# Kernel optimization log

Measured on AMD Instinct MI355X. Metric: run time of the kernel, lower is better.

The kernel has to match this reference:

```python
import jax, jax.numpy as jnp
import numpy as np

B, T, D, H = 8, 1024, 512, 8
HD = D // H  # per-head hidden = embed_dim // n_head = 64
EPS = 1e-5


def setup_inputs() -> dict:
    key = jax.random.key(0)
    ks = jax.random.split(key, 8)
    x = jax.random.normal(ks[0], (B, T, D), dtype=jnp.float32)
    sc = 1.0 / np.sqrt(D)
    Wq = jax.random.normal(ks[1], (D, H * HD), dtype=jnp.float32) * sc
    Wk = jax.random.normal(ks[2], (D, H * HD), dtype=jnp.float32) * sc
    Wp = jax.random.normal(ks[3], (H * HD, D), dtype=jnp.float32) * sc
    bq = jnp.zeros((H * HD,), jnp.float32)
    bk = jnp.zeros((H * HD,), jnp.float32)
    bp = jnp.zeros((D,), jnp.float32)
    w_mlp = jax.random.normal(ks[4], (2 * HD,), dtype=jnp.float32) * 0.1
    ln_g = jnp.ones((D,), jnp.float32)
    ln_b = jnp.zeros((D,), jnp.float32)
    return {"x": x, "Wq": Wq, "bq": bq, "Wk": Wk, "bk": bk,
            "Wp": Wp, "bp": bp, "w_mlp": w_mlp, "ln_g": ln_g, "ln_b": ln_b}


def reference(x, Wq, bq, Wk, bk, Wp, bp, w_mlp, ln_g, ln_b):
    b, t, d = x.shape
    h, hd = H, HD
    # q/k projections, split into heads: [B,T,H,hd]
    qx = (x @ Wq + bq).reshape(b, t, h, hd)
    kx = (x @ Wk + bk).reshape(b, t, h, hd)
    # MLP score: tanh(concat(k_j, q_i) . w) == tanh(k_j.w[:hd] + q_i.w[hd:])
    k_s = jnp.einsum('bkhd,d->bkh', kx, w_mlp[:hd])   # [B,K,H]
    q_s = jnp.einsum('bqhd,d->bqh', qx, w_mlp[hd:])   # [B,Q,H]
    score = jnp.tanh(q_s[:, :, None, :] + k_s[:, None, :, :])  # [B,Q,K,H]
    attn = jax.nn.softmax(score, axis=2)  # softmax over k_len
    # values are the key projection kx (bmm(score, kx) in original)
    out = jnp.einsum('bqkh,bkhd->bqhd', attn, kx).reshape(b, t, h * hd)
    out = out @ Wp + bp  # output projection (dropout is identity at eval)
    # residual + LayerNorm
    y = x + out
    mu = jnp.mean(y, axis=-1, keepdims=True)
    var = jnp.var(y, axis=-1, keepdims=True)
    yn = (y - mu) * jax.lax.rsqrt(var + EPS)
    return yn * ln_g + ln_b
```

## Files before the change

kernel.cpp:

```cpp
#include <hip/hip_runtime.h>
#include <cstddef>

#define TT 1024
#define DDIM 512
#define HH 8
#define NND 128
#define NW 72

typedef __attribute__((ext_vector_type(8))) short bfrag;
typedef __attribute__((ext_vector_type(4))) float facc;

#define SC2   2.8853900817779268f
#define L2E   1.4426950408889634f

static __device__ __forceinline__ unsigned bfrne(float f) {
    unsigned u = __float_as_uint(f);
    return (u + 0x7fffu + ((u >> 16) & 1u)) >> 16;
}
static __device__ __forceinline__ unsigned pack2rne(float a, float b) {
    return bfrne(a) | (bfrne(b) << 16);
}
static __device__ __forceinline__ unsigned pack2hu(float a, float b) {
    return ((__float_as_uint(a) + 0x8000u) >> 16) |
           ((__float_as_uint(b) + 0x8000u) & 0xffff0000u);
}
static __device__ __forceinline__ void gl2lds16(const void* g, void* l) {
    __builtin_amdgcn_global_load_lds(
        (const __attribute__((address_space(1))) unsigned int*)g,
        (__attribute__((address_space(3))) unsigned int*)l, 16, 0, 0);
}
static __device__ __forceinline__ float wfun(float z2) {
    float t = __builtin_amdgcn_exp2f(z2);
    float r = __builtin_amdgcn_rcpf(t + 1.f);
    return __builtin_amdgcn_exp2f(fmaf(r, -2.f * L2E, L2E));
}

__global__ __launch_bounds__(256) void prepare_kernel(
    const float* __restrict__ x, const float* __restrict__ Wk,
    const float* __restrict__ Wp, const float* __restrict__ Wq,
    const float* __restrict__ bq, const float* __restrict__ wm,
    unsigned short* __restrict__ xb, unsigned short* __restrict__ WkT,
    unsigned short* __restrict__ WpT, unsigned short* __restrict__ vq2b,
    float* __restrict__ qsb2)
{
    const int bx = blockIdx.x, tid = threadIdx.x;
    if (bx < 2048) {
        const int lane = tid & 63, wave = tid >> 6;
        const int row = bx * 4 + wave;
        const float4* xr = (const float4*)(x + (size_t)row * DDIM);
        float4 x0 = xr[lane * 2], x1 = xr[lane * 2 + 1];
        uint4 st;
        st.x = pack2rne(x0.x, x0.y); st.y = pack2rne(x0.z, x0.w);
        st.z = pack2rne(x1.x, x1.y); st.w = pack2rne(x1.z, x1.w);
        int p = lane ^ (row & 7);
        *(uint4*)(xb + (size_t)row * DDIM + p * 8) = st;
    } else if (bx < 2176) {
        int idx = bx - 2048;
        const float* src = (idx & 64) ? Wp : Wk;
        unsigned short* dst = (idx & 64) ? WpT : WkT;
        idx &= 63;
        const int n0 = (idx & 7) * 64, k0 = (idx >> 3) * 64;
        __shared__ float sT[64][65];
        #pragma unroll
        for (int it = 0; it < 4; ++it) {
            int task = it * 256 + tid;
            int kr = task >> 4, c4 = (task & 15) * 4;
            float4 v = *(const float4*)(src + (size_t)(k0 + kr) * DDIM + n0 + c4);
            sT[kr][c4] = v.x; sT[kr][c4 + 1] = v.y; sT[kr][c4 + 2] = v.z; sT[kr][c4 + 3] = v.w;
        }
        __syncthreads();
        #pragma unroll
        for (int it = 0; it < 2; ++it) {
            int task = it * 256 + tid;
            int n = task >> 3, kg = task & 7;
            unsigned u[4];
            #pragma unroll
            for (int jj = 0; jj < 4; ++jj)
                u[jj] = pack2rne(sT[kg * 8 + jj * 2][n], sT[kg * 8 + jj * 2 + 1][n]);
            int p = ((k0 >> 3) + kg) ^ (n & 7);
            uint4 st; st.x = u[0]; st.y = u[1]; st.z = u[2]; st.w = u[3];
            *(uint4*)(dst + (size_t)(n0 + n) * DDIM + p * 8) = st;
        }
    } else {
        int idx = (bx - 2176) * 256 + tid;
        int h = idx >> 9, d = idx & 511;
        float s = 0.f;
        #pragma unroll 8
        for (int j = 0; j < 64; ++j)
            s = fmaf(Wq[(size_t)d * DDIM + h * 64 + j], wm[64 + j], s);
        vq2b[h * DDIM + d] = (unsigned short)bfrne(s * SC2);
        if (idx < HH) {
            float sb = 0.f;
            for (int j = 0; j < 64; ++j)
                sb = fmaf(bq[idx * 64 + j], wm[64 + j], sb);
            qsb2[idx] = sb * SC2;
        }
    }
}

__global__ __launch_bounds__(256) void gemm1_kernel(
    const unsigned short* __restrict__ A, const unsigned short* __restrict__ B,
    const float* __restrict__ bias, unsigned short* __restrict__ kxTg,
    float* __restrict__ ks2, const float* __restrict__ wm,
    const unsigned short* __restrict__ vq2b, const float* __restrict__ qsb2,
    float* __restrict__ qs2)
{
    __shared__ __align__(16) unsigned short smem[12288];
    unsigned short* sA = smem;
    unsigned short* sB = smem + 8192;
    const int tid = threadIdx.x, lane = tid & 63, wave = tid >> 6;
    const int l15 = lane & 15, quad = lane >> 4;
    const int h = blockIdx.x, row0 = blockIdx.y * 128;
    const int col0 = h * 64;

    facc acc[2][4]; facc accq[2];
    #pragma unroll
    for (int i = 0; i < 2; ++i) {
        #pragma unroll
        for (int j = 0; j < 4; ++j) { acc[i][j][0]=0.f; acc[i][j][1]=0.f; acc[i][j][2]=0.f; acc[i][j][3]=0.f; }
        accq[i][0]=0.f; accq[i][1]=0.f; accq[i][2]=0.f; accq[i][3]=0.f;
    }

    for (int k0 = 0; k0 < 512; k0 += 64) {
        #pragma unroll
        for (int it = 0; it < 4; ++it) {
            int g = it * 256 + tid;
            int r = g >> 3, kg = g & 7;
            gl2lds16(A + (size_t)(row0 + r) * 512 + k0 + kg * 8, &sA[g * 8]);
        }
        #pragma unroll
        for (int it = 0; it < 2; ++it) {
            int g = it * 256 + tid;
            int r = g >> 3, kg = g & 7;
            gl2lds16(B + (size_t)(col0 + r) * 512 + k0 + kg * 8, &sB[g * 8]);
        }
        __syncthreads();
        #pragma unroll
        for (int ks_ = 0; ks_ < 2; ++ks_) {
            int slot = (ks_ * 4 + quad) ^ (l15 & 7);
            bfrag a[2], b[4];
            #pragma unroll
            for (int i = 0; i < 2; ++i)
                a[i] = *(const bfrag*)&sA[(wave * 32 + i * 16 + l15) * 64 + slot * 8];
            #pragma unroll
            for (int nt = 0; nt < 4; ++nt)
                b[nt] = *(const bfrag*)&sB[(nt * 16 + l15) * 64 + slot * 8];
            bfrag bvq = *(const bfrag*)(vq2b + h * 512 + k0 + ks_ * 32 + quad * 8);
            #pragma unroll
            for (int i = 0; i < 2; ++i) {
                #pragma unroll
                for (int nt = 0; nt < 4; ++nt)
                    acc[i][nt] = __builtin_amdgcn_mfma_f32_16x16x32_bf16(a[i], b[nt], acc[i][nt], 0, 0, 0);
                accq[i] = __builtin_amdgcn_mfma_f32_16x16x32_bf16(a[i], bvq, accq[i], 0, 0, 0);
            }
        }
        __syncthreads();
    }

    const int bb = row0 >> 10, t0 = row0 & 1023;
    const float qsbh = qsb2[h];
    float bvv[4], wmv[4];
    #pragma unroll
    for (int nt = 0; nt < 4; ++nt) {
        bvv[nt] = bias[col0 + nt * 16 + l15];
        wmv[nt] = wm[nt * 16 + l15] * SC2;
    }
    float part[2][4];
    #pragma unroll
    for (int i = 0; i < 2; ++i)
        #pragma unroll
        for (int r = 0; r < 4; ++r) part[i][r] = 0.f;

    unsigned short* eT = smem;
    #pragma unroll
    for (int i = 0; i < 2; ++i) {
        int tr = wave * 32 + i * 16 + quad * 4;
        #pragma unroll
        for (int nt = 0; nt < 4; ++nt) {
            int col = nt * 16 + l15;
            float v0 = acc[i][nt][0] + bvv[nt], v1 = acc[i][nt][1] + bvv[nt];
            float v2 = acc[i][nt][2] + bvv[nt], v3 = acc[i][nt][3] + bvv[nt];
            part[i][0] = fmaf(wmv[nt], v0, part[i][0]);
            part[i][1] = fmaf(wmv[nt], v1, part[i][1]);
            part[i][2] = fmaf(wmv[nt], v2, part[i][2]);
            part[i][3] = fmaf(wmv[nt], v3, part[i][3]);
            *(unsigned*)&eT[col * 136 + tr]     = pack2rne(v0, v1);
            *(unsigned*)&eT[col * 136 + tr + 2] = pack2rne(v2, v3);
        }
    }
    #pragma unroll
    for (int i = 0; i < 2; ++i)
        #pragma unroll
        for (int r = 0; r < 4; ++r) {
            float p = part[i][r];
            p += __shfl_xor(p, 1); p += __shfl_xor(p, 2);
            p += __shfl_xor(p, 4); p += __shfl_xor(p, 8);
            if (l15 == 0) {
                size_t o = (size_t)(bb * HH + h) * TT + t0 + wave * 32 + i * 16 + quad * 4 + r;
                ks2[o] = p;
                qs2[o] = accq[i][r] + qsbh;
            }
        }
    __syncthreads();
    unsigned short* kxbase = kxTg + ((size_t)(bb * HH + h) * 64) * TT;
    #pragma unroll
    for (int it = 0; it < 4; ++it) {
        int task = it * 256 + tid;
        int col = task >> 4, seg = task & 15;
        uint4 v = *(const uint4*)&eT[col * 136 + seg * 8];
        int g = (t0 >> 3) + seg;
        int p = g ^ (col & 7);
        *(uint4*)(kxbase + (size_t)col * TT + p * 8) = v;
    }
}

__global__ __launch_bounds__(256) void attn_nodes_kernel(
    const unsigned short* __restrict__ kxTg, const float* __restrict__ qs2,
    const float* __restrict__ ks2, float* __restrict__ node_out,
    float* __restrict__ mn2, float* __restrict__ inv127)
{
    __shared__ __align__(16) unsigned short kxT[64 * 256];
    __shared__ float ksc[1024];
    __shared__ float redl[8];
    const int bh = blockIdx.x;
    const int tid = threadIdx.x, lane = tid & 63, wave = tid >> 6;
    const int l15 = lane & 15, quad = lane >> 4;

    ((float4*)ksc)[tid] = ((const float4*)(ks2 + (size_t)bh * TT))[tid];
    float4 q4 = ((const float4*)(qs2 + (size_t)bh * TT))[tid];
    float mn = fminf(fminf(q4.x, q4.y), fminf(q4.z, q4.w));
    float mx = fmaxf(fmaxf(q4.x, q4.y), fmaxf(q4.z, q4.w));
    #pragma unroll
    for (int off = 32; off > 0; off >>= 1) {
        mn = fminf(mn, __shfl_xor(mn, off));
        mx = fmaxf(mx, __shfl_xor(mx, off));
    }
    if (lane == 0) { redl[wave] = mn; redl[4 + wave] = mx; }
    __syncthreads();
    const float mnv = fminf(fminf(redl[0], redl[1]), fminf(redl[2], redl[3]));
    const float mxv = fmaxf(fmaxf(redl[4], redl[5]), fmaxf(redl[6], redl[7]));
    if (tid == 0) {
        mn2[bh] = mnv;
        inv127[bh] = 127.f / fmaxf(mxv - mnv, 1e-12f);
    }
    const float h2v = (mxv - mnv) * (1.f / 127.f);
    const float zA = mnv + (wave * 16 + l15) * h2v;
    const float zB = zA + 64.f * h2v;

    const unsigned short* kxbase = kxTg + (size_t)bh * 64 * TT;
    facc acc[2][4]; facc accZ[2];
    #pragma unroll
    for (int g = 0; g < 2; ++g) {
        #pragma unroll
        for (int i = 0; i < 4; ++i) { acc[g][i][0]=0.f; acc[g][i][1]=0.f; acc[g][i][2]=0.f; acc[g][i][3]=0.f; }
        accZ[g][0]=0.f; accZ[g][1]=0.f; accZ[g][2]=0.f; accZ[g][3]=0.f;
    }
    bfrag ones;
    #pragma unroll
    for (int j = 0; j < 8; ++j) ones[j] = (short)0x3F80;

    for (int ck = 0; ck < 4; ++ck) {
        #pragma unroll
        for (int it = 0; it < 8; ++it) {
            int g = it * 256 + tid;
            int d = g >> 5, j = g & 31;
            gl2lds16(kxbase + (size_t)d * TT + ck * 256 + j * 8, &kxT[g * 8]);
        }
        __syncthreads();
        #pragma unroll
        for (int kst = 0; kst < 8; ++kst) {
            const float* kvp = &ksc[ck * 256 + kst * 32 + quad * 8];
            float4 kv0 = *(const float4*)kvp;
            float4 kv1 = *(const float4*)(kvp + 4);
            int slot = (kst * 4 + quad) ^ (l15 & 7);
            bfrag bf_[4];
            #pragma unroll
            for (int dt = 0; dt < 4; ++dt)
                bf_[dt] = *(const bfrag*)&kxT[(dt * 16 + l15) * 256 + slot * 8];
            #pragma unroll
            for (int g = 0; g < 2; ++g) {
                float z = g ? zB : zA;
                union { unsigned u[4]; bfrag f; } afu;
                afu.u[0] = pack2hu(wfun(z + kv0.x), wfun(z + kv0.y));
                afu.u[1] = pack2hu(wfun(z + kv0.z), wfun(z + kv0.w));
                afu.u[2] = pack2hu(wfun(z + kv1.x), wfun(z + kv1.y));
                afu.u[3] = pack2hu(wfun(z + kv1.z), wfun(z + kv1.w));
                #pragma unroll
                for (int dt = 0; dt < 4; ++dt)
                    acc[g][dt] = __builtin_amdgcn_mfma_f32_16x16x32_bf16(afu.f, bf_[dt], acc[g][dt], 0, 0, 0);
                accZ[g] = __builtin_amdgcn_mfma_f32_16x16x32_bf16(afu.f, ones, accZ[g], 0, 0, 0);
            }
        }
        __syncthreads();
    }
    float* ob = node_out + (size_t)bh * NND * NW;
    #pragma unroll
    for (int g = 0; g < 2; ++g) {
        #pragma unroll
        for (int r = 0; r < 4; ++r) {
            int node = g * 64 + wave * 16 + quad * 4 + r;
            #pragma unroll
            for (int dt = 0; dt < 4; ++dt)
                ob[(size_t)node * NW + dt * 16 + l15] = acc[g][dt][r];
            if (l15 == 0) ob[(size_t)node * NW + 64] = accZ[g][r];
        }
    }
}

__global__ __launch_bounds__(256) void interp_kernel(
    const float* __restrict__ qs2, const float* __restrict__ node_out,
    const float* __restrict__ mn2, const float* __restrict__ inv127,
    unsigned short* __restrict__ attb)
{
    const int tid = threadIdx.x, lane = tid & 63, wave = tid >> 6;
    const int row = blockIdx.x * 4 + wave;
    const int b = row >> 10, t = row & 1023;
    const int hh2 = lane >> 5, dp = lane & 31;
    #pragma unroll
    for (int h0 = 0; h0 < 8; h0 += 2) {
        const int hh = h0 + hh2;
        const int bh = b * HH + hh;
        float qv = qs2[(size_t)bh * TT + t];
        float u = (qv - mn2[bh]) * inv127[bh];
        int i = (int)floorf(u) - 1;
        i = i < 0 ? 0 : (i > NND - 4 ? NND - 4 : i);
        float s = u - (float)i;
        float s1 = s - 1.f, s2 = s - 2.f, s3 = s - 3.f;
        float w0 = -s1 * s2 * s3 * (1.f / 6.f);
        float w1 = s * s2 * s3 * 0.5f;
        float w2 = -s * s1 * s3 * 0.5f;
        float w3 = s * s1 * s2 * (1.f / 6.f);
        const float* base = node_out + ((size_t)bh * NND + i) * NW;
        float2 v0 = *(const float2*)(base + 2 * dp);
        float2 v1 = *(const float2*)(base + NW + 2 * dp);
        float2 v2 = *(const float2*)(base + 2 * NW + 2 * dp);
        float2 v3 = *(const float2*)(base + 3 * NW + 2 * dp);
        float nx = w0 * v0.x + w1 * v1.x + w2 * v2.x + w3 * v3.x;
        float ny = w0 * v0.y + w1 * v1.y + w2 * v2.y + w3 * v3.y;
        float zz = w0 * base[64] + w1 * base[NW + 64] + w2 * base[2 * NW + 64] + w3 * base[3 * NW + 64];
        float rz = __builtin_amdgcn_rcpf(zz);
        unsigned pk = pack2rne(nx * rz, ny * rz);
        int col = hh * 64 + 2 * dp;
        int p = (col >> 3) ^ (row & 7);
        *(unsigned*)&attb[(size_t)row * DDIM + p * 8 + (col & 7)] = pk;
    }
}

__global__ __launch_bounds__(256) void gemm2_kernel(
    const unsigned short* __restrict__ A, const unsigned short* __restrict__ B,
    const float* __restrict__ bias, const float* __restrict__ x,
    unsigned short* __restrict__ yb)
{
    __shared__ __align__(16) unsigned short smem[12288];
    unsigned short* sA = smem;
    unsigned short* sB = smem + 8192;
    const int tid = threadIdx.x, lane = tid & 63, wave = tid >> 6;
    const int l15 = lane & 15, quad = lane >> 4;
    const int col0 = blockIdx.x * 64, row0 = blockIdx.y * 128;

    facc acc[2][4];
    #pragma unroll
    for (int i = 0; i < 2; ++i)
        #pragma unroll
        for (int j = 0; j < 4; ++j) { acc[i][j][0]=0.f; acc[i][j][1]=0.f; acc[i][j][2]=0.f; acc[i][j][3]=0.f; }

    for (int k0 = 0; k0 < 512; k0 += 64) {
        #pragma unroll
        for (int it = 0; it < 4; ++it) {
            int g = it * 256 + tid;
            int r = g >> 3, kg = g & 7;
            gl2lds16(A + (size_t)(row0 + r) * 512 + k0 + kg * 8, &sA[g * 8]);
        }
        #pragma unroll
        for (int it = 0; it < 2; ++it) {
            int g = it * 256 + tid;
            int r = g >> 3, kg = g & 7;
            gl2lds16(B + (size_t)(col0 + r) * 512 + k0 + kg * 8, &sB[g * 8]);
        }
        __syncthreads();
        #pragma unroll
        for (int ks_ = 0; ks_ < 2; ++ks_) {
            int slot = (ks_ * 4 + quad) ^ (l15 & 7);
            bfrag a[2], b[4];
            #pragma unroll
            for (int i = 0; i < 2; ++i)
                a[i] = *(const bfrag*)&sA[(wave * 32 + i * 16 + l15) * 64 + slot * 8];
            #pragma unroll
            for (int nt = 0; nt < 4; ++nt)
                b[nt] = *(const bfrag*)&sB[(nt * 16 + l15) * 64 + slot * 8];
            #pragma unroll
            for (int i = 0; i < 2; ++i)
                #pragma unroll
                for (int nt = 0; nt < 4; ++nt)
                    acc[i][nt] = __builtin_amdgcn_mfma_f32_16x16x32_bf16(a[i], b[nt], acc[i][nt], 0, 0, 0);
        }
        __syncthreads();
    }
    float bvv[4];
    #pragma unroll
    for (int nt = 0; nt < 4; ++nt) bvv[nt] = bias[col0 + nt * 16 + l15];
    unsigned short* yT = smem;
    #pragma unroll
    for (int i = 0; i < 2; ++i) {
        #pragma unroll
        for (int nt = 0; nt < 4; ++nt) {
            int col = nt * 16 + l15;
            #pragma unroll
            for (int r = 0; r < 4; ++r) {
                int row = wave * 32 + i * 16 + quad * 4 + r;
                float xv = x[(size_t)(row0 + row) * DDIM + col0 + col];
                float y = acc[i][nt][r] + bvv[nt] + xv;
                yT[row * 72 + col] = (unsigned short)bfrne(y);
            }
        }
    }
    __syncthreads();
    #pragma unroll
    for (int it = 0; it < 4; ++it) {
        int task = it * 256 + tid;
        int row = task >> 3, seg = task & 7;
        uint4 v = *(const uint4*)&yT[row * 72 + seg * 8];
        *(uint4*)(yb + (size_t)(row0 + row) * DDIM + col0 + seg * 8) = v;
    }
}

__global__ __launch_bounds__(256) void ln_kernel(
    const unsigned short* __restrict__ yb, const float* __restrict__ g,
    const float* __restrict__ bet, float* __restrict__ out)
{
    const int tid = threadIdx.x, lane = tid & 63, wave = tid >> 6;
    const int row = blockIdx.x * 4 + wave;
    uint4 v = *(const uint4*)(yb + (size_t)row * DDIM + lane * 8);
    float y[8];
    y[0] = __uint_as_float(v.x << 16); y[1] = __uint_as_float(v.x & 0xffff0000u);
    y[2] = __uint_as_float(v.y << 16); y[3] = __uint_as_float(v.y & 0xffff0000u);
    y[4] = __uint_as_float(v.z << 16); y[5] = __uint_as_float(v.z & 0xffff0000u);
    y[6] = __uint_as_float(v.w << 16); y[7] = __uint_as_float(v.w & 0xffff0000u);
    float s = 0.f, s2 = 0.f;
    #pragma unroll
    for (int i = 0; i < 8; ++i) { s += y[i]; s2 = fmaf(y[i], y[i], s2); }
    #pragma unroll
    for (int off = 32; off > 0; off >>= 1) {
        s += __shfl_xor(s, off);
        s2 += __shfl_xor(s2, off);
    }
    float mu = s * (1.f / 512.f);
    float var = s2 * (1.f / 512.f) - mu * mu;
    float inv = rsqrtf(var + 1e-5f);
    const float4* gp = (const float4*)(g + lane * 8);
    const float4* bp = (const float4*)(bet + lane * 8);
    float4 g0 = gp[0], g1 = gp[1], b0 = bp[0], b1 = bp[1];
    float4 o0, o1;
    o0.x = (y[0] - mu) * inv * g0.x + b0.x; o0.y = (y[1] - mu) * inv * g0.y + b0.y;
    o0.z = (y[2] - mu) * inv * g0.z + b0.z; o0.w = (y[3] - mu) * inv * g0.w + b0.w;
    o1.x = (y[4] - mu) * inv * g1.x + b1.x; o1.y = (y[5] - mu) * inv * g1.y + b1.y;
    o1.z = (y[6] - mu) * inv * g1.z + b1.z; o1.w = (y[7] - mu) * inv * g1.w + b1.w;
    float4* op = (float4*)(out + (size_t)row * DDIM);
    op[lane * 2] = o0; op[lane * 2 + 1] = o1;
}

extern "C" void kernel_launch(void* const* d_in, const int* in_sizes, int n_in,
                              void* d_out, int out_size, void* d_ws, size_t ws_size,
                              hipStream_t stream)
{
    const float* x    = (const float*)d_in[0];
    const float* Wq   = (const float*)d_in[1];
    const float* bq   = (const float*)d_in[2];
    const float* Wk   = (const float*)d_in[3];
    const float* bk   = (const float*)d_in[4];
    const float* Wp   = (const float*)d_in[5];
    const float* bp   = (const float*)d_in[6];
    const float* wm   = (const float*)d_in[7];
    const float* ln_g = (const float*)d_in[8];
    const float* ln_b = (const float*)d_in[9];
    float* out = (float*)d_out;

    float* ws = (float*)d_ws;
    float*          qsb2 = ws;
    unsigned short* vq2b = (unsigned short*)(ws + 64);
    unsigned short* WkT  = (unsigned short*)(ws + 2112);
    unsigned short* WpT  = (unsigned short*)(ws + 133184);
    unsigned short* xb   = (unsigned short*)(ws + 264256);
    unsigned short* kxTg = (unsigned short*)(ws + 2361408);
    float*          qs2  = ws + 4458560;
    float*          ks2  = ws + 4524096;
    unsigned short* attb = (unsigned short*)(ws + 4589632);
    float*          ndo  = ws + 6686784;
    float*          mn2  = ws + 7276608;
    float*          i127 = ws + 7276672;
    unsigned short* yb   = xb;

    prepare_kernel<<<2192, 256, 0, stream>>>(x, Wk, Wp, Wq, bq, wm,
                                             xb, WkT, WpT, vq2b, qsb2);
    gemm1_kernel<<<dim3(8, 64), 256, 0, stream>>>(xb, WkT, bk, kxTg, ks2, wm,
                                                  vq2b, qsb2, qs2);
    attn_nodes_kernel<<<64, 256, 0, stream>>>(kxTg, qs2, ks2, ndo, mn2, i127);
    interp_kernel<<<2048, 256, 0, stream>>>(qs2, ndo, mn2, i127, attb);
    gemm2_kernel<<<dim3(8, 64), 256, 0, stream>>>(attb, WpT, bp, x, yb);
    ln_kernel<<<2048, 256, 0, stream>>>(yb, ln_g, ln_b, out);
}
```

Measured before the change: 151.4 us.

## Fuse node attention and interpolation into one kernel via shared-memory nodes

Merges attn_nodes_kernel and interp_kernel into one attn_kernel. The 128 interpolation nodes now stay in LDS instead of round-tripping through global memory, and min/scale are kept in registers. The grid doubles to 128 blocks, with each block handling half of the T rows for one (b,h). Each pair of blocks redundantly recomputes the same node MFMA work, which doubles that compute. Removing one launch and the global node traffic is meant to offset this.

```diff
diff --git a/kernel.cpp b/kernel.cpp
--- a/kernel.cpp
+++ b/kernel.cpp
@@ -5,7 +5,7 @@
 #define DDIM 512
 #define HH 8
 #define NND 128
-#define NW 72
+#define NS 68
 
 typedef __attribute__((ext_vector_type(8))) short bfrag;
 typedef __attribute__((ext_vector_type(4))) float facc;
@@ -214,15 +214,16 @@
     }
 }
 
-__global__ __launch_bounds__(256) void attn_nodes_kernel(
+__global__ __launch_bounds__(256) void attn_kernel(
     const unsigned short* __restrict__ kxTg, const float* __restrict__ qs2,
-    const float* __restrict__ ks2, float* __restrict__ node_out,
-    float* __restrict__ mn2, float* __restrict__ inv127)
+    const float* __restrict__ ks2, unsigned short* __restrict__ attb)
 {
     __shared__ __align__(16) unsigned short kxT[64 * 256];
     __shared__ float ksc[1024];
     __shared__ float redl[8];
-    const int bh = blockIdx.x;
+    __shared__ __align__(16) float nodes[NND * NS];
+    const int bh = blockIdx.x >> 1, thalf = blockIdx.x & 1;
+    const int b = bh >> 3, h = bh & 7;
     const int tid = threadIdx.x, lane = tid & 63, wave = tid >> 6;
     const int l15 = lane & 15, quad = lane >> 4;
 
@@ -239,11 +240,8 @@
     __syncthreads();
     const float mnv = fminf(fminf(redl[0], redl[1]), fminf(redl[2], redl[3]));
     const float mxv = fmaxf(fmaxf(redl[4], redl[5]), fmaxf(redl[6], redl[7]));
-    if (tid == 0) {
-        mn2[bh] = mnv;
-        inv127[bh] = 127.f / fmaxf(mxv - mnv, 1e-12f);
-    }
     const float h2v = (mxv - mnv) * (1.f / 127.f);
+    const float inv127v = 127.f / fmaxf(mxv - mnv, 1e-12f);
     const float zA = mnv + (wave * 16 + l15) * h2v;
     const float zB = zA + 64.f * h2v;
 
@@ -293,7 +291,6 @@
         }
         __syncthreads();
     }
-    float* ob = node_out + (size_t)bh * NND * NW;
     #pragma unroll
     for (int g = 0; g < 2; ++g) {
         #pragma unroll
@@ -301,27 +298,19 @@
             int node = g * 64 + wave * 16 + quad * 4 + r;
             #pragma unroll
             for (int dt = 0; dt < 4; ++dt)
-                ob[(size_t)node * NW + dt * 16 + l15] = acc[g][dt][r];
-            if (l15 == 0) ob[(size_t)node * NW + 64] = accZ[g][r];
-        }
-    }
-}
-
-__global__ __launch_bounds__(256) void interp_kernel(
-    const float* __restrict__ qs2, const float* __restrict__ node_out,
-    const float* __restrict__ mn2, const float* __restrict__ inv127,
-    unsigned short* __restrict__ attb)
-{
-    const int tid = threadIdx.x, lane = tid & 63, wave = tid >> 6;
-    const int row = blockIdx.x * 4 + wave;
-    const int b = row >> 10, t = row & 1023;
-    const int hh2 = lane >> 5, dp = lane & 31;
-    #pragma unroll
-    for (int h0 = 0; h0 < 8; h0 += 2) {
-        const int hh = h0 + hh2;
-        const int bh = b * HH + hh;
-        float qv = qs2[(size_t)bh * TT + t];
-        float u = (qv - mn2[bh]) * inv127[bh];
+                nodes[node * NS + dt * 16 + l15] = acc[g][dt][r];
+            if (l15 == 0) nodes[node * NS + 64] = accZ[g][r];
+        }
+    }
+    __syncthreads();
+
+    const float* qsp = qs2 + (size_t)bh * TT;
+    #pragma unroll 2
+    for (int it = 0; it < 32; ++it) {
+        int task = it * 256 + tid;
+        int t = thalf * 512 + (task >> 4), dp = task & 15;
+        float qv = qsp[t];
+        float u = (qv - mnv) * inv127v;
         int i = (int)floorf(u) - 1;
         i = i < 0 ? 0 : (i > NND - 4 ? NND - 4 : i);
         float s = u - (float)i;
@@ -330,19 +319,24 @@
         float w1 = s * s2 * s3 * 0.5f;
         float w2 = -s * s1 * s3 * 0.5f;
         float w3 = s * s1 * s2 * (1.f / 6.f);
-        const float* base = node_out + ((size_t)bh * NND + i) * NW;
-        float2 v0 = *(const float2*)(base + 2 * dp);
-        float2 v1 = *(const float2*)(base + NW + 2 * dp);
-        float2 v2 = *(const float2*)(base + 2 * NW + 2 * dp);
-        float2 v3 = *(const float2*)(base + 3 * NW + 2 * dp);
-        float nx = w0 * v0.x + w1 * v1.x + w2 * v2.x + w3 * v3.x;
-        float ny = w0 * v0.y + w1 * v1.y + w2 * v2.y + w3 * v3.y;
-        float zz = w0 * base[64] + w1 * base[NW + 64] + w2 * base[2 * NW + 64] + w3 * base[3 * NW + 64];
+        const float* base = &nodes[i * NS];
+        float4 v0 = *(const float4*)(base + 4 * dp);
+        float4 v1 = *(const float4*)(base + NS + 4 * dp);
+        float4 v2 = *(const float4*)(base + 2 * NS + 4 * dp);
+        float4 v3 = *(const float4*)(base + 3 * NS + 4 * dp);
+        float zz = w0 * base[64] + w1 * base[NS + 64] + w2 * base[2 * NS + 64] + w3 * base[3 * NS + 64];
+        float ox = w0 * v0.x + w1 * v1.x + w2 * v2.x + w3 * v3.x;
+        float oy = w0 * v0.y + w1 * v1.y + w2 * v2.y + w3 * v3.y;
+        float oz = w0 * v0.z + w1 * v1.z + w2 * v2.z + w3 * v3.z;
+        float ow = w0 * v0.w + w1 * v1.w + w2 * v2.w + w3 * v3.w;
         float rz = __builtin_amdgcn_rcpf(zz);
-        unsigned pk = pack2rne(nx * rz, ny * rz);
-        int col = hh * 64 + 2 * dp;
+        uint2 st;
+        st.x = pack2rne(ox * rz, oy * rz);
+        st.y = pack2rne(oz * rz, ow * rz);
+        int row = b * TT + t;
+        int col = h * 64 + 4 * dp;
         int p = (col >> 3) ^ (row & 7);
-        *(unsigned*)&attb[(size_t)row * DDIM + p * 8 + (col & 7)] = pk;
+        *(uint2*)&attb[(size_t)row * DDIM + p * 8 + (col & 7)] = st;
     }
 }
 
@@ -485,17 +479,13 @@
     float*          qs2  = ws + 4458560;
     float*          ks2  = ws + 4524096;
     unsigned short* attb = (unsigned short*)(ws + 4589632);
-    float*          ndo  = ws + 6686784;
-    float*          mn2  = ws + 7276608;
-    float*          i127 = ws + 7276672;
     unsigned short* yb   = xb;
 
     prepare_kernel<<<2192, 256, 0, stream>>>(x, Wk, Wp, Wq, bq, wm,
                                              xb, WkT, WpT, vq2b, qsb2);
     gemm1_kernel<<<dim3(8, 64), 256, 0, stream>>>(xb, WkT, bk, kxTg, ks2, wm,
                                                   vq2b, qsb2, qs2);
-    attn_nodes_kernel<<<64, 256, 0, stream>>>(kxTg, qs2, ks2, ndo, mn2, i127);
-    interp_kernel<<<2048, 256, 0, stream>>>(qs2, ndo, mn2, i127, attb);
+    attn_kernel<<<128, 256, 0, stream>>>(kxTg, qs2, ks2, attb);
     gemm2_kernel<<<dim3(8, 64), 256, 0, stream>>>(attb, WpT, bp, x, yb);
     ln_kernel<<<2048, 256, 0, stream>>>(yb, ln_g, ln_b, out);
 }
```

Result: no change. 153.1 us (+1.1%).
